# Kernel tuning notes

Measured on AMD Instinct MI355X. Metric: run time of the kernel, lower is better.

## Reference

```python
import jax, jax.numpy as jnp
import numpy as np

# dims: B scenes, V views, T tokens per view, D=d1=d2 embed dim, H=4*D mlp hidden
B, V, T, D = 2, 8, 512, 1024
H = 4 * D
LN_EPS = 1e-5


def setup_inputs() -> dict:
    key = jax.random.key(0)
    ks = jax.random.split(key, 9)
    x = jax.random.normal(ks[0], (B, V, T, D), jnp.float32)
    theta_Q = jax.random.normal(ks[1], (D, D), jnp.float32)  # Task.theta_Q ~ randn
    # TTT_MLP params (nn.Linear default-init scale approximated; exact dist irrelevant for math)
    W1 = jax.random.normal(ks[2], (D, H), jnp.float32) * (1.0 / np.sqrt(D))
    b1 = jnp.zeros((H,), jnp.float32)
    W2 = jax.random.normal(ks[3], (H, D), jnp.float32) * (1.0 / np.sqrt(H))
    b2 = jnp.zeros((D,), jnp.float32)
    gamma = jnp.ones((D,), jnp.float32)   # LayerNorm weight
    beta = jnp.zeros((D,), jnp.float32)   # LayerNorm bias
    alpha = jnp.full((1, D), 0.01, jnp.float32)
    return {"x": x, "theta_Q": theta_Q, "W1": W1, "b1": b1, "W2": W2,
            "b2": b2, "gamma": gamma, "beta": beta, "alpha": alpha}


def _layernorm(y, gamma, beta):
    mu = jnp.mean(y, axis=-1, keepdims=True)
    var = jnp.mean(jnp.square(y - mu), axis=-1, keepdims=True)  # biased, as torch LayerNorm
    return (y - mu) * jax.lax.rsqrt(var + LN_EPS) * gamma + beta


def reference(x, theta_Q, W1, b1, W2, b2, gamma, beta, alpha):
    # NOTE: in the original module, update_model rebinds a local (`p = p - lr*g`),
    # so the learner params are NEVER updated; proxy_loss/grads are dead code w.r.t.
    # the output. Faithful math: out = TTT_MLP(x @ theta_Q), fully parallel over tokens.
    z = jnp.einsum('bvtd,de->bvte', x, theta_Q)          # [B,V,T,D]
    h = jax.nn.gelu(z @ W1 + b1, approximate=False)      # exact erf GELU, as torch nn.GELU
    y = h @ W2 + b2                                      # [B,V,T,D]
    ln = _layernorm(y, gamma, beta)
    return z + jnp.tanh(alpha) * ln
```

## Files before the change

### kernel.cpp

```cpp
#include <hip/hip_runtime.h>
#include <hip/hip_bf16.h>
#include <cstdint>
#include <math.h>

typedef __hip_bfloat16 bf16_t;
typedef __attribute__((ext_vector_type(8))) __bf16 bf16x8;
typedef __attribute__((ext_vector_type(4))) float f32x4;

static_assert(sizeof(bf16x8) == 16, "bf16x8 must be 4 VGPRs");

static constexpr int DD = 1024;
static constexpr int HH = 4096;

#define GLD16(gp, lp)                                                                              \
  __builtin_amdgcn_global_load_lds(                                                                \
      (__attribute__((address_space(1))) void*)(uintptr_t)(gp),                                    \
      (__attribute__((address_space(3))) void*)(uint32_t)(uintptr_t)(lp), 16, 0, 0)

#if !__has_builtin(__builtin_amdgcn_exp2f)
#define __builtin_amdgcn_exp2f(x) exp2f(x)
#endif
#if !__has_builtin(__builtin_amdgcn_rcpf)
#define __builtin_amdgcn_rcpf(x) (1.0f / (x))
#endif

__device__ __forceinline__ float fast_gelu(float u) {
  const float t = __builtin_amdgcn_exp2f(-2.4554089f * u);
  return u * __builtin_amdgcn_rcpf(1.0f + t);
}

__global__ __launch_bounds__(256) void k_split_x(const float* __restrict__ x,
                                                 bf16_t* __restrict__ xh,
                                                 bf16_t* __restrict__ xl, int n4) {
  int i = blockIdx.x * 256 + threadIdx.x;
  const int stride = gridDim.x * 256;
  for (; i < n4; i += stride) {
    const float4 v = reinterpret_cast<const float4*>(x)[i];
    float vv[4] = {v.x, v.y, v.z, v.w};
    union { bf16_t b[4]; short4 s; } H, L;
#pragma unroll
    for (int j = 0; j < 4; ++j) {
      H.b[j] = __float2bfloat16(vv[j]);
      L.b[j] = __float2bfloat16(vv[j] - __bfloat162float(H.b[j]));
    }
    reinterpret_cast<short4*>(xh)[i] = H.s;
    reinterpret_cast<short4*>(xl)[i] = L.s;
  }
}

template <bool SPLIT>
__global__ __launch_bounds__(256) void k_transpose(const float* __restrict__ W,
                                                   bf16_t* __restrict__ Th,
                                                   bf16_t* __restrict__ Tl, int K, int N) {
  __shared__ float tile[32][33];
  const int n0 = blockIdx.x * 32, k0 = blockIdx.y * 32;
  const int tx = threadIdx.x, ty = threadIdx.y;
#pragma unroll
  for (int r = 0; r < 4; ++r) {
    const int k = ty + r * 8;
    tile[k][tx] = W[(size_t)(k0 + k) * N + n0 + tx];
  }
  __syncthreads();
#pragma unroll
  for (int r = 0; r < 4; ++r) {
    const int n = ty + r * 8;
    const float v = tile[tx][n];
    const bf16_t h = __float2bfloat16(v);
    Th[(size_t)(n0 + n) * K + k0 + tx] = h;
    if (SPLIT) Tl[(size_t)(n0 + n) * K + k0 + tx] = __float2bfloat16(v - __bfloat162float(h));
  }
}

template <int EPI, bool SPLIT>
__global__ __launch_bounds__(256) void k_gemm(const bf16_t* __restrict__ Ah,
                                              const bf16_t* __restrict__ Al,
                                              const bf16_t* __restrict__ BTh,
                                              const bf16_t* __restrict__ BTl,
                                              const float* __restrict__ bias,
                                              float* __restrict__ Cf,
                                              bf16_t* __restrict__ Cb, int M, int N, int K) {
  constexpr int BM = 128, BN = 128, BK = 32;
  __shared__ __align__(16) bf16_t sAh[BM * BK];
  __shared__ __align__(16) bf16_t sBh[BN * BK];
  __shared__ __align__(16) bf16_t sAl[SPLIT ? BM * BK : 8];
  __shared__ __align__(16) bf16_t sBl[SPLIT ? BN * BK : 8];

  const int nbn = N / BN;
  const int nwg = gridDim.x;
  const int wg = blockIdx.x;
  const int cpx = nwg >> 3;
  const int swz = (wg & 7) * cpx + (wg >> 3);
  const int bm = swz / nbn, bn = swz % nbn;

  const int t = threadIdx.x;
  const int l = t & 63;
  const int w = t >> 6;
  const int wr = (w >> 1) * 64, wc = (w & 1) * 64;

  const size_t Abase = (size_t)bm * BM * K;
  const size_t Bbase = (size_t)bn * BN * K;

  const int r0 = t >> 2, kc0 = (t & 3) * 8;
  const int r1 = r0 + 64;

  f32x4 acc[4][4] = {};
  const int lm = l & 15;
  const int kb8 = (l >> 4) * 8;

  const int nk = K / BK;
  for (int kt = 0; kt < nk; ++kt) {
    const size_t gk = (size_t)kt * BK;
    GLD16(Ah + Abase + (size_t)r0 * K + gk + kc0, &sAh[r0 * BK + kc0]);
    GLD16(Ah + Abase + (size_t)r1 * K + gk + kc0, &sAh[r1 * BK + kc0]);
    GLD16(BTh + Bbase + (size_t)r0 * K + gk + kc0, &sBh[r0 * BK + kc0]);
    GLD16(BTh + Bbase + (size_t)r1 * K + gk + kc0, &sBh[r1 * BK + kc0]);
    if (SPLIT) {
      GLD16(Al + Abase + (size_t)r0 * K + gk + kc0, &sAl[r0 * BK + kc0]);
      GLD16(Al + Abase + (size_t)r1 * K + gk + kc0, &sAl[r1 * BK + kc0]);
      GLD16(BTl + Bbase + (size_t)r0 * K + gk + kc0, &sBl[r0 * BK + kc0]);
      GLD16(BTl + Bbase + (size_t)r1 * K + gk + kc0, &sBl[r1 * BK + kc0]);
    }
    __syncthreads();

    bf16x8 a[4], b[4];
#pragma unroll
    for (int m = 0; m < 4; ++m)
      a[m] = *reinterpret_cast<const bf16x8*>(&sAh[(wr + m * 16 + lm) * BK + kb8]);
#pragma unroll
    for (int n = 0; n < 4; ++n)
      b[n] = *reinterpret_cast<const bf16x8*>(&sBh[(wc + n * 16 + lm) * BK + kb8]);
#pragma unroll
    for (int m = 0; m < 4; ++m)
#pragma unroll
      for (int n = 0; n < 4; ++n)
        acc[m][n] = __builtin_amdgcn_mfma_f32_16x16x32_bf16(a[m], b[n], acc[m][n], 0, 0, 0);

    if (SPLIT) {
      bf16x8 al_[4], bl_[4];
#pragma unroll
      for (int m = 0; m < 4; ++m)
        al_[m] = *reinterpret_cast<const bf16x8*>(&sAl[(wr + m * 16 + lm) * BK + kb8]);
#pragma unroll
      for (int n = 0; n < 4; ++n)
        bl_[n] = *reinterpret_cast<const bf16x8*>(&sBl[(wc + n * 16 + lm) * BK + kb8]);
#pragma unroll
      for (int m = 0; m < 4; ++m)
#pragma unroll
        for (int n = 0; n < 4; ++n) {
          acc[m][n] = __builtin_amdgcn_mfma_f32_16x16x32_bf16(a[m], bl_[n], acc[m][n], 0, 0, 0);
          acc[m][n] = __builtin_amdgcn_mfma_f32_16x16x32_bf16(al_[m], b[n], acc[m][n], 0, 0, 0);
        }
    }
    __syncthreads();
  }

  const int cr = (l >> 4) * 4;
#pragma unroll
  for (int m = 0; m < 4; ++m) {
#pragma unroll
    for (int n = 0; n < 4; ++n) {
      const int c = bn * BN + wc + n * 16 + lm;
      const float bc = (EPI == 2 || EPI == 3) ? bias[c] : 0.0f;
#pragma unroll
      for (int j = 0; j < 4; ++j) {
        const int r = bm * BM + wr + m * 16 + cr + j;
        const size_t idx = (size_t)r * N + c;
        const float v = acc[m][n][j];
        if (EPI == 1) {
          Cf[idx] = v;
          Cb[idx] = __float2bfloat16(v);
        } else if (EPI == 2) {
          Cb[idx] = __float2bfloat16(fast_gelu(v + bc));
        } else {
          Cf[idx] = v + bc;
        }
      }
    }
  }
}

__global__ __launch_bounds__(256) void k_ln_res(const float* __restrict__ y,
                                                const float* __restrict__ z,
                                                const float* __restrict__ gamma,
                                                const float* __restrict__ beta,
                                                const float* __restrict__ alpha,
                                                float* __restrict__ out) {
  const int row = blockIdx.x;
  const int t = threadIdx.x;
  const float4 v = reinterpret_cast<const float4*>(y + (size_t)row * DD)[t];
  float s = v.x + v.y + v.z + v.w;
  float q = v.x * v.x + v.y * v.y + v.z * v.z + v.w * v.w;
#pragma unroll
  for (int m = 1; m < 64; m <<= 1) {
    s += __shfl_xor(s, m, 64);
    q += __shfl_xor(q, m, 64);
  }
  __shared__ float ss[4], sq[4];
  if ((t & 63) == 0) { ss[t >> 6] = s; sq[t >> 6] = q; }
  __syncthreads();
  s = ss[0] + ss[1] + ss[2] + ss[3];
  q = sq[0] + sq[1] + sq[2] + sq[3];
  const float mu = s * (1.0f / DD);
  const float var = fmaxf(q * (1.0f / DD) - mu * mu, 0.0f);
  const float rs = rsqrtf(var + 1e-5f);
  const float4 g = reinterpret_cast<const float4*>(gamma)[t];
  const float4 bb = reinterpret_cast<const float4*>(beta)[t];
  const float4 aa = reinterpret_cast<const float4*>(alpha)[t];
  const float4 zz = reinterpret_cast<const float4*>(z + (size_t)row * DD)[t];
  float4 o;
  o.x = zz.x + tanhf(aa.x) * ((v.x - mu) * rs * g.x + bb.x);
  o.y = zz.y + tanhf(aa.y) * ((v.y - mu) * rs * g.y + bb.y);
  o.z = zz.z + tanhf(aa.z) * ((v.z - mu) * rs * g.z + bb.z);
  o.w = zz.w + tanhf(aa.w) * ((v.w - mu) * rs * g.w + bb.w);
  reinterpret_cast<float4*>(out + (size_t)row * DD)[t] = o;
}

extern "C" void kernel_launch(void* const* d_in, const int* in_sizes, int n_in, void* d_out,
                              int out_size, void* d_ws, size_t ws_size, hipStream_t stream) {
  const float* x   = (const float*)d_in[0];
  const float* thQ = (const float*)d_in[1];
  const float* W1  = (const float*)d_in[2];
  const float* b1  = (const float*)d_in[3];
  const float* W2  = (const float*)d_in[4];
  const float* b2  = (const float*)d_in[5];
  const float* gam = (const float*)d_in[6];
  const float* bet = (const float*)d_in[7];
  const float* alp = (const float*)d_in[8];
  float* out = (float*)d_out;

  const int M = in_sizes[0] / DD;

  char* ws = (char*)d_ws;
  size_t off = 0;
  auto take = [&](size_t bytes) -> char* {
    char* p = ws + off;
    off += (bytes + 255) & ~(size_t)255;
    return p;
  };
  bf16_t* xh  = (bf16_t*)take((size_t)M * DD * 2);
  bf16_t* xl  = (bf16_t*)take((size_t)M * DD * 2);
  bf16_t* qTh = (bf16_t*)take((size_t)DD * DD * 2);
  bf16_t* qTl = (bf16_t*)take((size_t)DD * DD * 2);
  bf16_t* w1T = (bf16_t*)take((size_t)DD * HH * 2);
  bf16_t* w2T = (bf16_t*)take((size_t)HH * DD * 2);
  float*  zf  = (float*)take((size_t)M * DD * 4);
  bf16_t* zb  = (bf16_t*)take((size_t)M * DD * 2);
  bf16_t* hb  = (bf16_t*)take((size_t)M * HH * 2);
  float*  yf  = (float*)take((size_t)M * DD * 4);

  hipLaunchKernelGGL(k_split_x, dim3(2048), dim3(256), 0, stream, x, xh, xl, M * DD / 4);
  hipLaunchKernelGGL((k_transpose<true>), dim3(DD / 32, DD / 32), dim3(32, 8), 0, stream,
                     thQ, qTh, qTl, DD, DD);
  hipLaunchKernelGGL((k_transpose<false>), dim3(HH / 32, DD / 32), dim3(32, 8), 0, stream,
                     W1, w1T, (bf16_t*)nullptr, DD, HH);
  hipLaunchKernelGGL((k_transpose<false>), dim3(DD / 32, HH / 32), dim3(32, 8), 0, stream,
                     W2, w2T, (bf16_t*)nullptr, HH, DD);

  hipLaunchKernelGGL((k_gemm<1, true>), dim3((M / 128) * (DD / 128)), dim3(256), 0, stream,
                     xh, xl, qTh, qTl, (const float*)nullptr, zf, zb, M, DD, DD);
  hipLaunchKernelGGL((k_gemm<2, false>), dim3((M / 128) * (HH / 128)), dim3(256), 0, stream,
                     zb, (const bf16_t*)nullptr, w1T, (const bf16_t*)nullptr, b1,
                     (float*)nullptr, hb, M, HH, DD);
  hipLaunchKernelGGL((k_gemm<3, false>), dim3((M / 128) * (DD / 128)), dim3(256), 0, stream,
                     hb, (const bf16_t*)nullptr, w2T, (const bf16_t*)nullptr, b2,
                     yf, (bf16_t*)nullptr, M, DD, HH);
  hipLaunchKernelGGL(k_ln_res, dim3(M), dim3(256), 0, stream, yf, zf, gam, bet, alp, out);
}
```

Before: 399.3 us.

## Use BK=64 swizzled LDS tiles and split-K the W2 GEMM

Adds a BK=64 path to the GEMM with XOR-swizzled LDS layout for the two bf16-only GEMMs, halving barrier count per K. The W2 GEMM (K=4096, only 128 tiles) is split into two K halves written to separate fp32 buffers, raising the workgroup count to fill the GPU. The LayerNorm kernel then sums the two partials plus b2. The cost is an extra fp32 partial buffer write and read, and more LDS per workgroup, which may lower occupancy.

```diff
diff --git a/kernel.cpp b/kernel.cpp
--- a/kernel.cpp
+++ b/kernel.cpp
@@ -71,15 +71,17 @@
   }
 }
 
-template <int EPI, bool SPLIT>
+template <int EPI, bool SPLIT, int BK>
 __global__ __launch_bounds__(256) void k_gemm(const bf16_t* __restrict__ Ah,
                                               const bf16_t* __restrict__ Al,
                                               const bf16_t* __restrict__ BTh,
                                               const bf16_t* __restrict__ BTl,
                                               const float* __restrict__ bias,
                                               float* __restrict__ Cf,
-                                              bf16_t* __restrict__ Cb, int M, int N, int K) {
-  constexpr int BM = 128, BN = 128, BK = 32;
+                                              bf16_t* __restrict__ Cb,
+                                              int M, int N, int K, int LDK) {
+  static_assert(!SPLIT || BK == 32, "SPLIT path only implemented for BK=32");
+  constexpr int BM = 128, BN = 128;
   __shared__ __align__(16) bf16_t sAh[BM * BK];
   __shared__ __align__(16) bf16_t sBh[BN * BK];
   __shared__ __align__(16) bf16_t sAl[SPLIT ? BM * BK : 8];
@@ -92,75 +94,120 @@
   const int swz = (wg & 7) * cpx + (wg >> 3);
   const int bm = swz / nbn, bn = swz % nbn;
 
+  const int ks = blockIdx.y;
+  const size_t k0 = (size_t)ks * K;
+  Cf += (size_t)ks * M * N;
+
   const int t = threadIdx.x;
   const int l = t & 63;
   const int w = t >> 6;
   const int wr = (w >> 1) * 64, wc = (w & 1) * 64;
 
-  const size_t Abase = (size_t)bm * BM * K;
-  const size_t Bbase = (size_t)bn * BN * K;
-
-  const int r0 = t >> 2, kc0 = (t & 3) * 8;
-  const int r1 = r0 + 64;
+  const size_t Abase = (size_t)bm * BM * LDK + k0;
+  const size_t Bbase = (size_t)bn * BN * LDK + k0;
 
   f32x4 acc[4][4] = {};
   const int lm = l & 15;
-  const int kb8 = (l >> 4) * 8;
+  const int l4 = l >> 4;
 
   const int nk = K / BK;
   for (int kt = 0; kt < nk; ++kt) {
     const size_t gk = (size_t)kt * BK;
-    GLD16(Ah + Abase + (size_t)r0 * K + gk + kc0, &sAh[r0 * BK + kc0]);
-    GLD16(Ah + Abase + (size_t)r1 * K + gk + kc0, &sAh[r1 * BK + kc0]);
-    GLD16(BTh + Bbase + (size_t)r0 * K + gk + kc0, &sBh[r0 * BK + kc0]);
-    GLD16(BTh + Bbase + (size_t)r1 * K + gk + kc0, &sBh[r1 * BK + kc0]);
-    if (SPLIT) {
-      GLD16(Al + Abase + (size_t)r0 * K + gk + kc0, &sAl[r0 * BK + kc0]);
-      GLD16(Al + Abase + (size_t)r1 * K + gk + kc0, &sAl[r1 * BK + kc0]);
-      GLD16(BTl + Bbase + (size_t)r0 * K + gk + kc0, &sBl[r0 * BK + kc0]);
-      GLD16(BTl + Bbase + (size_t)r1 * K + gk + kc0, &sBl[r1 * BK + kc0]);
+    if (BK == 32) {
+      const int r0 = t >> 2, kc0 = (t & 3) * 8;
+      const int r1 = r0 + 64;
+      GLD16(Ah + Abase + (size_t)r0 * LDK + gk + kc0, &sAh[r0 * BK + kc0]);
+      GLD16(Ah + Abase + (size_t)r1 * LDK + gk + kc0, &sAh[r1 * BK + kc0]);
+      GLD16(BTh + Bbase + (size_t)r0 * LDK + gk + kc0, &sBh[r0 * BK + kc0]);
+      GLD16(BTh + Bbase + (size_t)r1 * LDK + gk + kc0, &sBh[r1 * BK + kc0]);
+      if (SPLIT) {
+        GLD16(Al + Abase + (size_t)r0 * LDK + gk + kc0, &sAl[r0 * BK + kc0]);
+        GLD16(Al + Abase + (size_t)r1 * LDK + gk + kc0, &sAl[r1 * BK + kc0]);
+        GLD16(BTl + Bbase + (size_t)r0 * LDK + gk + kc0, &sBl[r0 * BK + kc0]);
+        GLD16(BTl + Bbase + (size_t)r1 * LDK + gk + kc0, &sBl[r1 * BK + kc0]);
+      }
+    } else {
+#pragma unroll
+      for (int p = 0; p < 4; ++p) {
+        const int c = t + 256 * p;
+        const int r = c >> 3, j = c & 7;
+        const int jg = (j ^ (r & 7)) * 8;
+        GLD16(Ah + Abase + (size_t)r * LDK + gk + jg, &sAh[c * 8]);
+      }
+#pragma unroll
+      for (int p = 0; p < 4; ++p) {
+        const int c = t + 256 * p;
+        const int r = c >> 3, j = c & 7;
+        const int jg = (j ^ (r & 7)) * 8;
+        GLD16(BTh + Bbase + (size_t)r * LDK + gk + jg, &sBh[c * 8]);
+      }
     }
     __syncthreads();
 
-    bf16x8 a[4], b[4];
-#pragma unroll
-    for (int m = 0; m < 4; ++m)
-      a[m] = *reinterpret_cast<const bf16x8*>(&sAh[(wr + m * 16 + lm) * BK + kb8]);
-#pragma unroll
-    for (int n = 0; n < 4; ++n)
-      b[n] = *reinterpret_cast<const bf16x8*>(&sBh[(wc + n * 16 + lm) * BK + kb8]);
-#pragma unroll
-    for (int m = 0; m < 4; ++m)
+    if (BK == 32) {
+      const int kb8 = l4 * 8;
+      bf16x8 a[4], b[4];
+#pragma unroll
+      for (int m = 0; m < 4; ++m)
+        a[m] = *reinterpret_cast<const bf16x8*>(&sAh[(wr + m * 16 + lm) * BK + kb8]);
 #pragma unroll
       for (int n = 0; n < 4; ++n)
-        acc[m][n] = __builtin_amdgcn_mfma_f32_16x16x32_bf16(a[m], b[n], acc[m][n], 0, 0, 0);
-
-    if (SPLIT) {
-      bf16x8 al_[4], bl_[4];
+        b[n] = *reinterpret_cast<const bf16x8*>(&sBh[(wc + n * 16 + lm) * BK + kb8]);
 #pragma unroll
       for (int m = 0; m < 4; ++m)
-        al_[m] = *reinterpret_cast<const bf16x8*>(&sAl[(wr + m * 16 + lm) * BK + kb8]);
-#pragma unroll
-      for (int n = 0; n < 4; ++n)
-        bl_[n] = *reinterpret_cast<const bf16x8*>(&sBl[(wc + n * 16 + lm) * BK + kb8]);
-#pragma unroll
-      for (int m = 0; m < 4; ++m)
+#pragma unroll
+        for (int n = 0; n < 4; ++n)
+          acc[m][n] = __builtin_amdgcn_mfma_f32_16x16x32_bf16(a[m], b[n], acc[m][n], 0, 0, 0);
+
+      if (SPLIT) {
+        bf16x8 al_[4], bl_[4];
+#pragma unroll
+        for (int m = 0; m < 4; ++m)
+          al_[m] = *reinterpret_cast<const bf16x8*>(&sAl[(wr + m * 16 + lm) * BK + kb8]);
+#pragma unroll
+        for (int n = 0; n < 4; ++n)
+          bl_[n] = *reinterpret_cast<const bf16x8*>(&sBl[(wc + n * 16 + lm) * BK + kb8]);
+#pragma unroll
+        for (int m = 0; m < 4; ++m)
+#pragma unroll
+          for (int n = 0; n < 4; ++n) {
+            acc[m][n] = __builtin_amdgcn_mfma_f32_16x16x32_bf16(a[m], bl_[n], acc[m][n], 0, 0, 0);
+            acc[m][n] = __builtin_amdgcn_mfma_f32_16x16x32_bf16(al_[m], b[n], acc[m][n], 0, 0, 0);
+          }
+      }
+    } else {
+#pragma unroll
+      for (int h = 0; h < 2; ++h) {
+        bf16x8 a[4], b[4];
+#pragma unroll
+        for (int m = 0; m < 4; ++m) {
+          const int R = wr + m * 16 + lm;
+          const int q = (l4 + 4 * h) ^ (R & 7);
+          a[m] = *reinterpret_cast<const bf16x8*>(&sAh[R * 64 + q * 8]);
+        }
 #pragma unroll
         for (int n = 0; n < 4; ++n) {
-          acc[m][n] = __builtin_amdgcn_mfma_f32_16x16x32_bf16(a[m], bl_[n], acc[m][n], 0, 0, 0);
-          acc[m][n] = __builtin_amdgcn_mfma_f32_16x16x32_bf16(al_[m], b[n], acc[m][n], 0, 0, 0);
+          const int R = wc + n * 16 + lm;
+          const int q = (l4 + 4 * h) ^ (R & 7);
+          b[n] = *reinterpret_cast<const bf16x8*>(&sBh[R * 64 + q * 8]);
         }
+#pragma unroll
+        for (int m = 0; m < 4; ++m)
+#pragma unroll
+          for (int n = 0; n < 4; ++n)
+            acc[m][n] = __builtin_amdgcn_mfma_f32_16x16x32_bf16(a[m], b[n], acc[m][n], 0, 0, 0);
+      }
     }
     __syncthreads();
   }
 
-  const int cr = (l >> 4) * 4;
+  const int cr = l4 * 4;
 #pragma unroll
   for (int m = 0; m < 4; ++m) {
 #pragma unroll
     for (int n = 0; n < 4; ++n) {
       const int c = bn * BN + wc + n * 16 + lm;
-      const float bc = (EPI == 2 || EPI == 3) ? bias[c] : 0.0f;
+      const float bc = (EPI == 2) ? bias[c] : 0.0f;
 #pragma unroll
       for (int j = 0; j < 4; ++j) {
         const int r = bm * BM + wr + m * 16 + cr + j;
@@ -172,14 +219,16 @@
         } else if (EPI == 2) {
           Cb[idx] = __float2bfloat16(fast_gelu(v + bc));
         } else {
-          Cf[idx] = v + bc;
+          Cf[idx] = v;
         }
       }
     }
   }
 }
 
-__global__ __launch_bounds__(256) void k_ln_res(const float* __restrict__ y,
+__global__ __launch_bounds__(256) void k_ln_res(const float* __restrict__ y0,
+                                                const float* __restrict__ y1,
+                                                const float* __restrict__ b2,
                                                 const float* __restrict__ z,
                                                 const float* __restrict__ gamma,
                                                 const float* __restrict__ beta,
@@ -187,7 +236,12 @@
                                                 float* __restrict__ out) {
   const int row = blockIdx.x;
   const int t = threadIdx.x;
-  const float4 v = reinterpret_cast<const float4*>(y + (size_t)row * DD)[t];
+  const float4 va = reinterpret_cast<const float4*>(y0 + (size_t)row * DD)[t];
+  const float4 vb = reinterpret_cast<const float4*>(y1 + (size_t)row * DD)[t];
+  const float4 bc = reinterpret_cast<const float4*>(b2)[t];
+  float4 v;
+  v.x = va.x + vb.x + bc.x; v.y = va.y + vb.y + bc.y;
+  v.z = va.z + vb.z + bc.z; v.w = va.w + vb.w + bc.w;
   float s = v.x + v.y + v.z + v.w;
   float q = v.x * v.x + v.y * v.y + v.z * v.z + v.w * v.w;
 #pragma unroll
@@ -246,7 +300,7 @@
   float*  zf  = (float*)take((size_t)M * DD * 4);
   bf16_t* zb  = (bf16_t*)take((size_t)M * DD * 2);
   bf16_t* hb  = (bf16_t*)take((size_t)M * HH * 2);
-  float*  yf  = (float*)take((size_t)M * DD * 4);
+  float*  yf  = (float*)take((size_t)M * DD * 4 * 2);
 
   hipLaunchKernelGGL(k_split_x, dim3(2048), dim3(256), 0, stream, x, xh, xl, M * DD / 4);
   hipLaunchKernelGGL((k_transpose<true>), dim3(DD / 32, DD / 32), dim3(32, 8), 0, stream,
@@ -256,13 +310,14 @@
   hipLaunchKernelGGL((k_transpose<false>), dim3(DD / 32, HH / 32), dim3(32, 8), 0, stream,
                      W2, w2T, (bf16_t*)nullptr, HH, DD);
 
-  hipLaunchKernelGGL((k_gemm<1, true>), dim3((M / 128) * (DD / 128)), dim3(256), 0, stream,
-                     xh, xl, qTh, qTl, (const float*)nullptr, zf, zb, M, DD, DD);
-  hipLaunchKernelGGL((k_gemm<2, false>), dim3((M / 128) * (HH / 128)), dim3(256), 0, stream,
+  hipLaunchKernelGGL((k_gemm<1, true, 32>), dim3((M / 128) * (DD / 128)), dim3(256), 0, stream,
+                     xh, xl, qTh, qTl, (const float*)nullptr, zf, zb, M, DD, DD, DD);
+  hipLaunchKernelGGL((k_gemm<2, false, 64>), dim3((M / 128) * (HH / 128)), dim3(256), 0, stream,
                      zb, (const bf16_t*)nullptr, w1T, (const bf16_t*)nullptr, b1,
-                     (float*)nullptr, hb, M, HH, DD);
-  hipLaunchKernelGGL((k_gemm<3, false>), dim3((M / 128) * (DD / 128)), dim3(256), 0, stream,
-                     hb, (const bf16_t*)nullptr, w2T, (const bf16_t*)nullptr, b2,
-                     yf, (bf16_t*)nullptr, M, DD, HH);
-  hipLaunchKernelGGL(k_ln_res, dim3(M), dim3(256), 0, stream, yf, zf, gam, bet, alp, out);
-}
+                     (float*)nullptr, hb, M, HH, DD, DD);
+  hipLaunchKernelGGL((k_gemm<3, false, 64>), dim3((M / 128) * (DD / 128), 2), dim3(256), 0,
+                     stream, hb, (const bf16_t*)nullptr, w2T, (const bf16_t*)nullptr,
+                     (const float*)nullptr, yf, (bf16_t*)nullptr, M, DD, HH / 2, HH);
+  hipLaunchKernelGGL(k_ln_res, dim3(M), dim3(256), 0, stream,
+                     yf, yf + (size_t)M * DD, b2, zf, gam, bet, alp, out);
+}
```

New measurement: 389.8 us. 1.02x faster.
